# Kernel tuning notes

Measured on AMD Instinct MI355X. Metric: run time of the kernel, lower is better.

Reference implementation:

```python
import jax, jax.numpy as jnp
import numpy as np

N, D = 16384, 128

def setup_inputs() -> dict:
    key = jax.random.key(0)
    k1, k2 = jax.random.split(key)
    x = jax.random.normal(k1, (N, D), dtype=jnp.float32)
    adj = jax.random.randint(k2, (N, N), 0, 2, dtype=jnp.int32)
    return {"x": x, "adj": adj}

def reference(x, adj):
    # out[i] = x[i] + sum_{j: adj[i,j]==1} x[j]  ==  (adj + I) @ x
    a = adj.astype(x.dtype)
    return x + jnp.matmul(a, x)  # [N, D]
```

## Files before the change

### kernel.cpp

```cpp
#include <hip/hip_runtime.h>
#include <hip/hip_bf16.h>

#define GN 16384
#define GD 128
#define KSPLIT 4
#define KBLK (GN / KSPLIT)
#define PHK 128
#define NPH (KBLK / PHK)
#define NSTEP (PHK / 32)
#define BUF_SHORTS (GD * PHK)
#define OUT_ELEMS (GN * GD)
#define GNW (GN / 32)

typedef __attribute__((ext_vector_type(8))) short short8;
typedef __attribute__((ext_vector_type(4))) float floatx4;
typedef __attribute__((ext_vector_type(4))) int intx4;
typedef __attribute__((ext_vector_type(4))) unsigned uintx4;

static __device__ __forceinline__ unsigned short f32_to_bf16(float f) {
  unsigned u = __builtin_bit_cast(unsigned, f);
  unsigned r = u + 0x7FFFu + ((u >> 16) & 1u);
  return (unsigned short)(r >> 16);
}

__global__ __launch_bounds__(256) void prep_kernel(const float* __restrict__ x,
                                                   unsigned short* __restrict__ xT) {
  __shared__ unsigned short t[GD][66];
  const int tid = threadIdx.x;
  const int j0 = blockIdx.x * 64;
  for (int i = tid; i < 64 * GD; i += 256) {
    int j = i >> 7, d = i & (GD - 1);
    t[d][j] = f32_to_bf16(x[(size_t)(j0 + j) * GD + d]);
  }
  __syncthreads();
  for (int i = tid; i < GD * 32; i += 256) {
    int d = i >> 5, jp = i & 31;
    unsigned lo = t[d][2 * jp], hi = t[d][2 * jp + 1];
    *reinterpret_cast<unsigned*>(xT + (size_t)d * GN + j0 + 2 * jp) = lo | (hi << 16);
  }
}

__global__ __launch_bounds__(256) void pack_kernel(const int* __restrict__ adj,
                                                   unsigned* __restrict__ ubits) {
  const size_t total = (size_t)GN * GNW;
  size_t idx = (size_t)blockIdx.x * 256 + threadIdx.x;
  const size_t stride = (size_t)gridDim.x * 256;
  for (; idx < total; idx += stride) {
    const int* p = adj + idx * 32;
    unsigned res = 0;
#pragma unroll
    for (int j = 0; j < 8; ++j) {
      intx4 r = *(const intx4*)(p + j * 4);
      unsigned n = (unsigned)(r.x | (r.y << 1) | (r.z << 2) | (r.w << 3));
      res |= n << (4 * j);
    }
    ubits[idx] = res;
  }
}

__global__ __launch_bounds__(512, 4) void gemm_kernel(const unsigned* __restrict__ ubits,
                                                      const unsigned short* __restrict__ xT,
                                                      float* __restrict__ partials) {
  __shared__ unsigned short bbuf[2][BUF_SHORTS];
  const int tid = threadIdx.x;
  const int wave = tid >> 6;
  const int lane = tid & 63;
  const int q = lane >> 4;
  const int m = lane & 15;
  const int rbase = blockIdx.x * 128 + wave * 16;
  const int ks = blockIdx.y;
  const int kbase = ks * KBLK;

  const unsigned short* gptr[4];
  unsigned short* lptr[4];
#pragma unroll
  for (int p = 0; p < 4; ++p) {
    int s = tid + 512 * p;
    int n = s >> 4;
    int gsrc = (s & 15) ^ (n & 7);
    gptr[p] = xT + (size_t)n * GN + kbase + gsrc * 8;
    lptr[p] = &bbuf[0][0] + (size_t)s * 8;
  }

#define STAGE(bufsel, koff)                                                             \
  do {                                                                                  \
    _Pragma("unroll") for (int p = 0; p < 4; ++p) {                                     \
      __builtin_amdgcn_global_load_lds(                                                 \
          (const __attribute__((address_space(1))) unsigned int*)(gptr[p] + (koff)),    \
          (__attribute__((address_space(3))) unsigned int*)(lptr[p] +                   \
                                                           (bufsel) * BUF_SHORTS),      \
          16, 0, 0);                                                                    \
    }                                                                                   \
  } while (0)

  const unsigned* ub = ubits + (size_t)(rbase + m) * GNW + (kbase >> 5);

  floatx4 acc[8];
#pragma unroll
  for (int c = 0; c < 8; ++c) acc[c] = (floatx4){0.f, 0.f, 0.f, 0.f};

  STAGE(0, 0);
  uintx4 cw = *(const uintx4*)(ub);

  int buf = 0;
  for (int ph = 0; ph < NPH; ++ph) {
    __syncthreads();
    uintx4 nw;
    if (ph + 1 < NPH) {
      STAGE(buf ^ 1, (ph + 1) * PHK);
      nw = *(const uintx4*)(ub + (size_t)(ph + 1) * 4);
    }

#pragma unroll
    for (int st = 0; st < NSTEP; ++st) {
      short8 bf[8];
      const unsigned short* bb = &bbuf[buf][0] + (((st * 4 + q) ^ (m & 7)) * 8);
#pragma unroll
      for (int cc = 0; cc < 8; ++cc)
        bf[cc] = *(const short8*)(bb + (cc * 16 + m) * PHK);

      const unsigned w = cw[st];
      const unsigned b = (w >> (q * 8)) & 0xFFu;
      intx4 pk;
#pragma unroll
      for (int j = 0; j < 4; ++j) {
        unsigned t = (b >> (2 * j)) & 3u;
        pk[j] = (int)(((t * 0x8001u) & 0x10001u) * 0x3F80u);
      }
      const short8 af = __builtin_bit_cast(short8, pk);

#pragma unroll
      for (int cc = 0; cc < 8; ++cc)
        acc[cc] = __builtin_amdgcn_mfma_f32_16x16x32_bf16(af, bf[cc], acc[cc], 0, 0, 0);
    }

    cw = nw;
    buf ^= 1;
  }

  float* pp = partials + (size_t)ks * OUT_ELEMS + (size_t)rbase * GD;
#pragma unroll
  for (int cc = 0; cc < 8; ++cc)
#pragma unroll
    for (int r = 0; r < 4; ++r)
      pp[(size_t)(q * 4 + r) * GD + cc * 16 + m] = acc[cc][r];
}

__global__ __launch_bounds__(256) void reduce_kernel(const float* __restrict__ x,
                                                     const float* __restrict__ partials,
                                                     float* __restrict__ out) {
  size_t i = ((size_t)blockIdx.x * 256 + threadIdx.x) * 4;
  floatx4 v = *(const floatx4*)(x + i);
  v += *(const floatx4*)(partials + 0 * (size_t)OUT_ELEMS + i);
  v += *(const floatx4*)(partials + 1 * (size_t)OUT_ELEMS + i);
  v += *(const floatx4*)(partials + 2 * (size_t)OUT_ELEMS + i);
  v += *(const floatx4*)(partials + 3 * (size_t)OUT_ELEMS + i);
  *(floatx4*)(out + i) = v;
}

extern "C" void kernel_launch(void* const* d_in, const int* in_sizes, int n_in,
                              void* d_out, int out_size, void* d_ws, size_t ws_size,
                              hipStream_t stream) {
  const float* x = (const float*)d_in[0];
  const int* adj = (const int*)d_in[1];
  float* out = (float*)d_out;
  unsigned short* xT = (unsigned short*)d_ws;
  float* partials = (float*)((char*)d_ws + (size_t)GN * GD * 2);
  unsigned* ubits = (unsigned*)((char*)d_ws + (size_t)GN * GD * 2 +
                                (size_t)KSPLIT * OUT_ELEMS * 4);

  prep_kernel<<<GN / 64, 256, 0, stream>>>(x, xT);
  pack_kernel<<<2048, 256, 0, stream>>>(adj, ubits);
  gemm_kernel<<<dim3(GN / 128, KSPLIT), 512, 0, stream>>>(ubits, xT, partials);
  reduce_kernel<<<OUT_ELEMS / 4 / 256, 256, 0, stream>>>(x, partials, out);
}
```

Measured before the change: 1.431 ms.

## Retile GEMM waves to 64x32 tiles and stage adj packing through LDS

The GEMM kernel's eight waves are rearranged from each owning 16 rows by 128 columns into a 2x4 grid of 64x32 tiles. This cuts LDS B-fragment reads per wave (2 instead of 8 per step) and reuses them across 4 A-fragments. The adjacency bitmask words are now loaded at the start of each phase rather than prefetched one phase ahead. The pack kernel now stages adjacency rows into LDS through async global_load_lds with a swizzle, replacing per-thread strided 128-byte loads. This is meant to improve coalescing on the dominant 1 GiB adj read, at the cost of an explicit vmcnt wait.

```diff
diff --git a/kernel.cpp b/kernel.cpp
--- a/kernel.cpp
+++ b/kernel.cpp
@@ -42,19 +42,37 @@
 
 __global__ __launch_bounds__(256) void pack_kernel(const int* __restrict__ adj,
                                                    unsigned* __restrict__ ubits) {
-  const size_t total = (size_t)GN * GNW;
-  size_t idx = (size_t)blockIdx.x * 256 + threadIdx.x;
-  const size_t stride = (size_t)gridDim.x * 256;
-  for (; idx < total; idx += stride) {
-    const int* p = adj + idx * 32;
-    unsigned res = 0;
+  __shared__ int sb[4][2048];
+  const int tid = threadIdx.x;
+  const int wave = tid >> 6;
+  const int lane = tid & 63;
+  const int NITER = (GN * GNW) / 64;
+
+  int* const sw = &sb[wave][0];
+  int witer = blockIdx.x * 4 + wave;
+  const int wstride = gridDim.x * 4;
+  for (; witer < NITER; witer += wstride) {
+    const int* base = adj + (size_t)witer * 2048;
 #pragma unroll
     for (int j = 0; j < 8; ++j) {
-      intx4 r = *(const intx4*)(p + j * 4);
-      unsigned n = (unsigned)(r.x | (r.y << 1) | (r.z << 2) | (r.w << 3));
-      res |= n << (4 * j);
+      int idx = j * 64 + lane;
+      int l = idx >> 3, g = idx & 7;
+      int G = l * 8 + (g ^ (l & 7));
+      __builtin_amdgcn_global_load_lds(
+          (const __attribute__((address_space(1))) unsigned int*)(base + G * 4),
+          (__attribute__((address_space(3))) unsigned int*)(sw + idx * 4), 16, 0, 0);
     }
-    ubits[idx] = res;
+    asm volatile("s_waitcnt vmcnt(0)" ::: "memory");
+    unsigned out = 0;
+#pragma unroll
+    for (int j = 0; j < 8; ++j) {
+      intx4 r = *(const intx4*)(sw + lane * 32 + ((j ^ (lane & 7)) * 4));
+      unsigned nib = (unsigned)((r.x & 1) | ((r.y & 1) << 1) | ((r.z & 1) << 2) |
+                                ((r.w & 1) << 3));
+      out |= nib << (4 * j);
+    }
+    ubits[(size_t)witer * 64 + lane] = out;
+    asm volatile("" ::: "memory");
   }
 }
 
@@ -64,10 +82,11 @@
   __shared__ unsigned short bbuf[2][BUF_SHORTS];
   const int tid = threadIdx.x;
   const int wave = tid >> 6;
+  const int wr = wave >> 2;
+  const int wc = wave & 3;
   const int lane = tid & 63;
   const int q = lane >> 4;
   const int m = lane & 15;
-  const int rbase = blockIdx.x * 128 + wave * 16;
   const int ks = blockIdx.y;
   const int kbase = ks * KBLK;
 
@@ -93,57 +112,63 @@
     }                                                                                   \
   } while (0)
 
-  const unsigned* ub = ubits + (size_t)(rbase + m) * GNW + (kbase >> 5);
-
-  floatx4 acc[8];
-#pragma unroll
-  for (int c = 0; c < 8; ++c) acc[c] = (floatx4){0.f, 0.f, 0.f, 0.f};
+  const unsigned* ubp =
+      ubits + (size_t)(blockIdx.x * 128 + wr * 64 + m) * GNW + (kbase >> 5);
+
+  const int bshift = (wc * 32 + m) * PHK;
+  int swz8[NSTEP];
+#pragma unroll
+  for (int st = 0; st < NSTEP; ++st) swz8[st] = ((st * 4 + q) ^ (m & 7)) * 8;
+
+  floatx4 acc[4][2];
+#pragma unroll
+  for (int mt = 0; mt < 4; ++mt)
+#pragma unroll
+    for (int cc = 0; cc < 2; ++cc) acc[mt][cc] = (floatx4){0.f, 0.f, 0.f, 0.f};
 
   STAGE(0, 0);
-  uintx4 cw = *(const uintx4*)(ub);
 
   int buf = 0;
   for (int ph = 0; ph < NPH; ++ph) {
     __syncthreads();
-    uintx4 nw;
-    if (ph + 1 < NPH) {
-      STAGE(buf ^ 1, (ph + 1) * PHK);
-      nw = *(const uintx4*)(ub + (size_t)(ph + 1) * 4);
+    uintx4 cw[4];
+#pragma unroll
+    for (int mt = 0; mt < 4; ++mt)
+      cw[mt] = *(const uintx4*)(ubp + (size_t)mt * (16 * GNW) + ph * 4);
+    if (ph + 1 < NPH) STAGE(buf ^ 1, (ph + 1) * PHK);
+
+    const unsigned short* bb = &bbuf[buf][0] + bshift;
+#pragma unroll
+    for (int st = 0; st < NSTEP; ++st) {
+      short8 bf0 = *(const short8*)(bb + swz8[st]);
+      short8 bf1 = *(const short8*)(bb + 16 * PHK + swz8[st]);
+#pragma unroll
+      for (int mt = 0; mt < 4; ++mt) {
+        const unsigned b = (cw[mt][st] >> (q * 8)) & 0xFFu;
+        const unsigned n0 = b & 0xFu, n1 = b >> 4;
+        const unsigned w0 = n0 * 0x8001u, w1 = n1 * 0x8001u;
+        intx4 pk;
+        pk.x = (int)((w0 & 0x10001u) * 0x3F80u);
+        pk.y = (int)(((w0 >> 2) & 0x10001u) * 0x3F80u);
+        pk.z = (int)((w1 & 0x10001u) * 0x3F80u);
+        pk.w = (int)(((w1 >> 2) & 0x10001u) * 0x3F80u);
+        const short8 af = __builtin_bit_cast(short8, pk);
+        acc[mt][0] = __builtin_amdgcn_mfma_f32_16x16x32_bf16(af, bf0, acc[mt][0], 0, 0, 0);
+        acc[mt][1] = __builtin_amdgcn_mfma_f32_16x16x32_bf16(af, bf1, acc[mt][1], 0, 0, 0);
+      }
     }
-
-#pragma unroll
-    for (int st = 0; st < NSTEP; ++st) {
-      short8 bf[8];
-      const unsigned short* bb = &bbuf[buf][0] + (((st * 4 + q) ^ (m & 7)) * 8);
-#pragma unroll
-      for (int cc = 0; cc < 8; ++cc)
-        bf[cc] = *(const short8*)(bb + (cc * 16 + m) * PHK);
-
-      const unsigned w = cw[st];
-      const unsigned b = (w >> (q * 8)) & 0xFFu;
-      intx4 pk;
-#pragma unroll
-      for (int j = 0; j < 4; ++j) {
-        unsigned t = (b >> (2 * j)) & 3u;
-        pk[j] = (int)(((t * 0x8001u) & 0x10001u) * 0x3F80u);
-      }
-      const short8 af = __builtin_bit_cast(short8, pk);
-
-#pragma unroll
-      for (int cc = 0; cc < 8; ++cc)
-        acc[cc] = __builtin_amdgcn_mfma_f32_16x16x32_bf16(af, bf[cc], acc[cc], 0, 0, 0);
-    }
-
-    cw = nw;
     buf ^= 1;
   }
 
-  float* pp = partials + (size_t)ks * OUT_ELEMS + (size_t)rbase * GD;
-#pragma unroll
-  for (int cc = 0; cc < 8; ++cc)
-#pragma unroll
-    for (int r = 0; r < 4; ++r)
-      pp[(size_t)(q * 4 + r) * GD + cc * 16 + m] = acc[cc][r];
+  float* pp = partials + (size_t)ks * OUT_ELEMS + (size_t)(blockIdx.x * 128) * GD;
+#pragma unroll
+  for (int mt = 0; mt < 4; ++mt)
+#pragma unroll
+    for (int cc = 0; cc < 2; ++cc)
+#pragma unroll
+      for (int r = 0; r < 4; ++r)
+        pp[(size_t)(wr * 64 + mt * 16 + q * 4 + r) * GD + wc * 32 + cc * 16 + m] =
+            acc[mt][cc][r];
 }
 
 __global__ __launch_bounds__(256) void reduce_kernel(const float* __restrict__ x,
```

Result: slower. 1.466 ms (+2.4%).
